# Performance work log

Measured on AMD Instinct MI355X. Metric: run time of the kernel, lower is better.

The kernel has to match this reference:

```python
import jax, jax.numpy as jnp
import numpy as np

C = 1024
H = 16
D = C // H

def setup_inputs() -> dict:
    key = jax.random.key(0)
    ks = jax.random.split(key, 12)
    s = 1.0 / np.sqrt(C)
    inp = {
        "Q": jax.random.normal(ks[0], (2, 1024, C), jnp.float32),
        "K_in": jax.random.normal(ks[1], (2, 4096, C), jnp.float32),
        "V_in": jax.random.normal(ks[2], (2, 4096, C), jnp.float32),
        "V_bias": jax.random.normal(ks[3], (2, 4096), jnp.float32),
        "Wq_w": jax.random.uniform(ks[4], (C, C), jnp.float32, -s, s),
        "Wq_b": jax.random.uniform(ks[5], (C,), jnp.float32, -s, s),
        "Wk_w": jax.random.uniform(ks[6], (C, C), jnp.float32, -s, s),
        "Wk_b": jax.random.uniform(ks[7], (C,), jnp.float32, -s, s),
        "Wv_w": jax.random.uniform(ks[8], (C, C), jnp.float32, -s, s),
        "Wv_b": jax.random.uniform(ks[9], (C,), jnp.float32, -s, s),
        "Wo_w": jax.random.uniform(ks[10], (C, C), jnp.float32, -s, s),
        "Wo_b": jax.random.uniform(ks[11], (C,), jnp.float32, -s, s),
    }
    return inp

def reference(Q, K_in, V_in, V_bias, Wq_w, Wq_b, Wk_w, Wk_b, Wv_w, Wv_b, Wo_w, Wo_b):
    B, Lq, _ = Q.shape
    Lk = K_in.shape[1]
    # linear projections (torch Linear: x @ W.T + b), split heads -> [B,H,L,D]
    q = (Q @ Wq_w.T + Wq_b).reshape(B, Lq, H, D).transpose(0, 2, 1, 3)
    k = (K_in @ Wk_w.T + Wk_b).reshape(B, Lk, H, D).transpose(0, 2, 1, 3)
    v = (V_in @ Wv_w.T + Wv_b).reshape(B, Lk, H, D).transpose(0, 2, 1, 3)
    scale = 1.0 / np.sqrt(D).astype(np.float32)
    logits = jnp.einsum("bhqd,bhkd->bhqk", q, k) * scale
    logits = logits + V_bias[:, None, None, :]  # per-key additive bias
    attn = jax.nn.softmax(logits, axis=-1)      # dropout p=0.0 (eval)
    out = jnp.einsum("bhqk,bhkd->bhqd", attn, v)
    out = out.transpose(0, 2, 1, 3).reshape(B, Lq, C)
    return out @ Wo_w.T + Wo_b
```

## Files before the change

kernel.cpp:

```cpp
#include <hip/hip_runtime.h>


typedef __attribute__((ext_vector_type(8))) __bf16 bf16x8;
typedef __attribute__((ext_vector_type(4))) float f32x4;
typedef __attribute__((ext_vector_type(16))) float f32x16;

#define LOG2E 1.44269504f

__device__ __forceinline__ unsigned short f2bf(float f) {
  union { float f; unsigned u; } v; v.f = f;
  unsigned r = v.u + 0x7fffu + ((v.u >> 16) & 1u);
  return (unsigned short)(r >> 16);
}

__device__ __forceinline__ f32x4 mfma16(bf16x8 a, bf16x8 b, f32x4 c) {
  return __builtin_amdgcn_mfma_f32_16x16x32_bf16(a, b, c, 0, 0, 0);
}
__device__ __forceinline__ f32x16 mfma32(bf16x8 a, bf16x8 b, f32x16 c) {
  return __builtin_amdgcn_mfma_f32_32x32x16_bf16(a, b, c, 0, 0, 0);
}

__device__ __forceinline__ unsigned pk2(float lo, float hi) {
  unsigned short a = __builtin_bit_cast(unsigned short, (__bf16)lo);
  unsigned short b = __builtin_bit_cast(unsigned short, (__bf16)hi);
  return (unsigned)a | ((unsigned)b << 16);
}

struct Cvt4 {
  const float* src[4];
  unsigned short* dst[4];
};

__global__ __launch_bounds__(256) void cvt4_kernel(Cvt4 a, int n4) {
  const float4* s = (const float4*)a.src[blockIdx.y];
  unsigned short* d = a.dst[blockIdx.y];
  int stride = gridDim.x * blockDim.x;
  for (int i = blockIdx.x * blockDim.x + threadIdx.x; i < n4; i += stride) {
    float4 f = s[i];
    ushort4 u;
    u.x = f2bf(f.x); u.y = f2bf(f.y); u.z = f2bf(f.z); u.w = f2bf(f.w);
    ((ushort4*)d)[i] = u;
  }
}

template <int MODE, bool AF32>
__global__ __launch_bounds__(256) void gemm_bf16(
    const void* __restrict__ Ap, const unsigned short* __restrict__ W,
    const float* __restrict__ bias, void* __restrict__ outp,
    int M, int Llog2, float oscale) {
  constexpr int K = 1024, N = 1024;
  __shared__ unsigned short Alds[128][40];
  __shared__ unsigned short Blds[128][40];

  const int tid = threadIdx.x;
  const int wid = tid >> 6, l = tid & 63;
  const int wr = wid >> 1, wc = wid & 1;
  const int m0 = blockIdx.x * 128, n0 = blockIdx.y * 128;
  const int lg = l >> 4, lm = l & 15;

  const int crow = tid >> 2;
  const int ck8 = (tid & 3) * 8;

  const float* Af = (const float*)Ap;
  const unsigned short* Ab = (const unsigned short*)Ap;

  f32x4 acc[4][4] = {};
  uint4 ra[2], rb[2];

  auto loadA = [&](int kt, int half) -> uint4 {
    const int row = crow + half * 64;
    const long off = (long)(m0 + row) * K + kt * 32 + ck8;
    if constexpr (AF32) {
      float4 f0 = *(const float4*)(Af + off);
      float4 f1 = *(const float4*)(Af + off + 4);
      bf16x8 v;
      v[0] = (__bf16)f0.x; v[1] = (__bf16)f0.y;
      v[2] = (__bf16)f0.z; v[3] = (__bf16)f0.w;
      v[4] = (__bf16)f1.x; v[5] = (__bf16)f1.y;
      v[6] = (__bf16)f1.z; v[7] = (__bf16)f1.w;
      uint4 u;
      __builtin_memcpy(&u, &v, 16);
      return u;
    } else {
      return *(const uint4*)(Ab + off);
    }
  };
  auto loadB = [&](int kt, int half) -> uint4 {
    const int row = crow + half * 64;
    return *(const uint4*)(W + (long)(n0 + row) * K + kt * 32 + ck8);
  };

  ra[0] = loadA(0, 0); ra[1] = loadA(0, 1);
  rb[0] = loadB(0, 0); rb[1] = loadB(0, 1);

  for (int kt = 0; kt < K / 32; ++kt) {
    __syncthreads();
    *(uint4*)&Alds[crow][ck8] = ra[0];
    *(uint4*)&Alds[crow + 64][ck8] = ra[1];
    *(uint4*)&Blds[crow][ck8] = rb[0];
    *(uint4*)&Blds[crow + 64][ck8] = rb[1];
    __syncthreads();
    if (kt + 1 < K / 32) {
      ra[0] = loadA(kt + 1, 0); ra[1] = loadA(kt + 1, 1);
      rb[0] = loadB(kt + 1, 0); rb[1] = loadB(kt + 1, 1);
    }
    bf16x8 af[4], bfr[4];
#pragma unroll
    for (int i = 0; i < 4; ++i)
      af[i] = *(const bf16x8*)&Alds[wr * 64 + i * 16 + lm][lg * 8];
#pragma unroll
    for (int j = 0; j < 4; ++j)
      bfr[j] = *(const bf16x8*)&Blds[wc * 64 + j * 16 + lm][lg * 8];
#pragma unroll
    for (int i = 0; i < 4; ++i)
#pragma unroll
      for (int j = 0; j < 4; ++j) {
        if constexpr (MODE == 1)
          acc[i][j] = mfma16(bfr[i], af[j], acc[i][j]);
        else
          acc[i][j] = mfma16(af[i], bfr[j], acc[i][j]);
      }
  }

  const int rr = lg * 4;
  if constexpr (MODE == 0) {
    const int Lmask = (1 << Llog2) - 1;
    unsigned short* out = (unsigned short*)outp;
#pragma unroll
    for (int j = 0; j < 4; ++j) {
      const int n = n0 + wc * 64 + j * 16 + lm;
      const float bv = bias[n];
      const int h = n >> 6, d = n & 63;
#pragma unroll
      for (int i = 0; i < 4; ++i)
#pragma unroll
        for (int r = 0; r < 4; ++r) {
          const int m = m0 + wr * 64 + i * 16 + rr + r;
          const int b = m >> Llog2, li = m & Lmask;
          const long o = (((long)(b * 16 + h) << Llog2) + li) * 64 + d;
          out[o] = f2bf((acc[i][j][r] + bv) * oscale);
        }
    }
  } else if constexpr (MODE == 1) {
    unsigned short* out = (unsigned short*)outp;
#pragma unroll
    for (int i = 0; i < 4; ++i)
#pragma unroll
      for (int r = 0; r < 4; ++r) {
        const int n = n0 + wc * 64 + i * 16 + rr + r;
        const float bv = bias[n];
        const int h = n >> 6, d = n & 63;
#pragma unroll
        for (int j = 0; j < 4; ++j) {
          const int m = m0 + wr * 64 + j * 16 + lm;
          const int b = m >> 12, lk = m & 4095;
          const long o = ((long)((b * 16 + h) * 64 + d)) * 4096 + lk;
          out[o] = f2bf(acc[i][j][r] + bv);
        }
      }
  } else {
    float* out = (float*)outp;
#pragma unroll
    for (int j = 0; j < 4; ++j) {
      const int n = n0 + wc * 64 + j * 16 + lm;
      const float bv = bias[n];
#pragma unroll
      for (int i = 0; i < 4; ++i)
#pragma unroll
        for (int r = 0; r < 4; ++r) {
          const int m = m0 + wr * 64 + i * 16 + rr + r;
          out[(long)m * N + n] = acc[i][j][r] + bv;
        }
    }
  }
}

__global__ __launch_bounds__(256, 2) void attn32(
    const unsigned short* __restrict__ qh, const unsigned short* __restrict__ kh,
    const unsigned short* __restrict__ vT, const float* __restrict__ Vb,
    float* __restrict__ Opart, float* __restrict__ ml) {
  __shared__ unsigned short Klds[2][64][64];
  __shared__ unsigned short Vlds[2][64][64];

  const int tid = threadIdx.x;
  const int wid = tid >> 6, lane = tid & 63;
  const int lq = lane & 31;
  const int hi = lane >> 5;
  const int bh = blockIdx.x;
  const int qb = blockIdx.y;
  const int sp = blockIdx.z;
  const int b = bh >> 4;
  const int q = qb * 128 + wid * 32 + lq;
  const int kt0 = sp * 32;

  bf16x8 qr[4];
  {
    const unsigned short* qp = qh + ((long)bh * 1024 + q) * 64 + hi * 8;
#pragma unroll
    for (int dc = 0; dc < 4; ++dc) qr[dc] = *(const bf16x8*)(qp + dc * 16);
  }

  const int srow = tid >> 2;
  const int ss0 = (tid & 3) * 2, ss1 = ss0 + 1;
  const int sswz = srow & 7;
  const int kgrow = (srow & 0x33) | ((srow & 4) << 1) | ((srow & 8) >> 1);
  const unsigned short* kgp =
      kh + ((long)bh * 4096 + kt0 * 64 + kgrow) * 64;
  const unsigned short* vgp =
      vT + ((long)bh * 64 + srow) * 4096 + kt0 * 64;
  const int ko0 = (ss0 ^ sswz) * 8, ko1 = (ss1 ^ sswz) * 8;
  const float* bp = Vb + b * 4096 + kt0 * 64 + hi * 8;

  uint4 kr0, kr1, vr0, vr1;
  auto loadKV = [&](int t) {
    kr0 = *(const uint4*)(kgp + (long)t * 4096 + ko0);
    kr1 = *(const uint4*)(kgp + (long)t * 4096 + ko1);
    vr0 = *(const uint4*)(vgp + t * 64 + ko0);
    vr1 = *(const uint4*)(vgp + t * 64 + ko1);
  };
  loadKV(0);

  const int rsw = lq & 7;
  float mreg = -1e30f, lreg = 0.f;
  f32x16 oa0 = {}, oa1 = {};

  for (int t = 0; t < 32; ++t) {
    const int buf = t & 1;
    *(uint4*)&Klds[buf][srow][ss0 * 8] = kr0;
    *(uint4*)&Klds[buf][srow][ss1 * 8] = kr1;
    *(uint4*)&Vlds[buf][srow][ss0 * 8] = vr0;
    *(uint4*)&Vlds[buf][srow][ss1 * 8] = vr1;
    if (t + 1 < 32) loadKV(t + 1);

    float bvv[32];
#pragma unroll
    for (int kb = 0; kb < 2; ++kb)
#pragma unroll
      for (int g = 0; g < 4; ++g) {
        float4 t4 = *(const float4*)(bp + t * 64 + kb * 32 + (g & 1) * 4 +
                                     (g >> 1) * 16);
        const int o = kb * 16 + g * 4;
        bvv[o] = t4.x; bvv[o + 1] = t4.y; bvv[o + 2] = t4.z; bvv[o + 3] = t4.w;
      }

    __syncthreads();

    f32x16 sa0 = {}, sa1 = {};
#pragma unroll
    for (int dc = 0; dc < 4; ++dc) {
      const int w16 = dc * 2 + hi;
      bf16x8 kf0 = *(const bf16x8*)&Klds[buf][lq][(w16 ^ rsw) * 8];
      bf16x8 kf1 = *(const bf16x8*)&Klds[buf][32 + lq][(w16 ^ rsw) * 8];
      sa0 = mfma32(kf0, qr[dc], sa0);
      sa1 = mfma32(kf1, qr[dc], sa1);
    }

    float p[32];
#pragma unroll
    for (int r = 0; r < 16; ++r) p[r] = fmaf(bvv[r], LOG2E, sa0[r]);
#pragma unroll
    for (int r = 0; r < 16; ++r) p[16 + r] = fmaf(bvv[16 + r], LOG2E, sa1[r]);

    float t16[16];
#pragma unroll
    for (int i = 0; i < 16; ++i) t16[i] = fmaxf(p[i], p[i + 16]);
#pragma unroll
    for (int s = 8; s > 0; s >>= 1)
#pragma unroll
      for (int i = 0; i < 8; ++i)
        if (i < s) t16[i] = fmaxf(t16[i], t16[i + s]);
    float mx = fmaxf(t16[0], __shfl_xor(t16[0], 32));
    const float mnew = fmaxf(mreg, mx);
    const float al = __builtin_amdgcn_exp2f(mreg - mnew);
    mreg = mnew;
#pragma unroll
    for (int i = 0; i < 32; ++i) p[i] = __builtin_amdgcn_exp2f(p[i] - mreg);
    float s16[16];
#pragma unroll
    for (int i = 0; i < 16; ++i) s16[i] = p[i] + p[i + 16];
#pragma unroll
    for (int s = 8; s > 0; s >>= 1)
#pragma unroll
      for (int i = 0; i < 8; ++i)
        if (i < s) s16[i] += s16[i + s];
    float sm = s16[0] + __shfl_xor(s16[0], 32);
    lreg = lreg * al + sm;
#pragma unroll
    for (int r = 0; r < 16; ++r) { oa0[r] *= al; oa1[r] *= al; }

#pragma unroll
    for (int kc = 0; kc < 4; ++kc) {
      union { uint4 u; bf16x8 v; } pu;
      pu.u = make_uint4(pk2(p[kc * 8 + 0], p[kc * 8 + 1]),
                        pk2(p[kc * 8 + 2], p[kc * 8 + 3]),
                        pk2(p[kc * 8 + 4], p[kc * 8 + 5]),
                        pk2(p[kc * 8 + 6], p[kc * 8 + 7]));
      const int w16 = kc * 2 + hi;
      bf16x8 vf0 = *(const bf16x8*)&Vlds[buf][lq][(w16 ^ rsw) * 8];
      bf16x8 vf1 = *(const bf16x8*)&Vlds[buf][32 + lq][(w16 ^ rsw) * 8];
      oa0 = mfma32(vf0, pu.v, oa0);
      oa1 = mfma32(vf1, pu.v, oa1);
    }
    __syncthreads();
  }

  float* ob = Opart + (((long)sp * 32 + bh) * 1024 + q) * 64;
#pragma unroll
  for (int g = 0; g < 4; ++g) {
    *(float4*)(ob + g * 8 + hi * 4) =
        make_float4(oa0[g * 4], oa0[g * 4 + 1], oa0[g * 4 + 2], oa0[g * 4 + 3]);
    *(float4*)(ob + 32 + g * 8 + hi * 4) =
        make_float4(oa1[g * 4], oa1[g * 4 + 1], oa1[g * 4 + 2], oa1[g * 4 + 3]);
  }
  if (hi == 0)
    *(float2*)(ml + ((long)sp * 32 + bh) * 2048 + q * 2) =
        make_float2(mreg, lreg);
}

__global__ __launch_bounds__(256) void combine_kernel(
    const float* __restrict__ Opart, const float* __restrict__ ml,
    unsigned short* __restrict__ ao) {
  const int idx = blockIdx.x * 256 + threadIdx.x;
  const int bh = idx >> 10, q = idx & 1023;
  const int b = bh >> 4, h = bh & 15;
  const float2 a0 = *(const float2*)(ml + (long)idx * 2);
  const float2 a1 = *(const float2*)(ml + ((long)32768 + idx) * 2);
  const float mm = fmaxf(a0.x, a1.x);
  const float e0 = __builtin_amdgcn_exp2f(a0.x - mm);
  const float e1 = __builtin_amdgcn_exp2f(a1.x - mm);
  const float inv = 1.0f / (a0.y * e0 + a1.y * e1);
  const float s0 = e0 * inv, s1 = e1 * inv;
  const float* O0 = Opart + (long)idx * 64;
  const float* O1 = Opart + ((long)32768 + idx) * 64;
  unsigned short* op = ao + ((long)b * 1024 + q) * 1024 + h * 64;
#pragma unroll
  for (int d = 0; d < 64; d += 4) {
    float4 x = *(const float4*)(O0 + d);
    float4 y = *(const float4*)(O1 + d);
    ushort4 u;
    u.x = f2bf(x.x * s0 + y.x * s1);
    u.y = f2bf(x.y * s0 + y.y * s1);
    u.z = f2bf(x.z * s0 + y.z * s1);
    u.w = f2bf(x.w * s0 + y.w * s1);
    *(ushort4*)(op + d) = u;
  }
}

extern "C" void kernel_launch(void* const* d_in, const int* in_sizes, int n_in,
                              void* d_out, int out_size, void* d_ws,
                              size_t ws_size, hipStream_t stream) {
  const float* Q = (const float*)d_in[0];
  const float* K_in = (const float*)d_in[1];
  const float* V_in = (const float*)d_in[2];
  const float* V_bias = (const float*)d_in[3];
  const float* Wq_w = (const float*)d_in[4];
  const float* Wq_b = (const float*)d_in[5];
  const float* Wk_w = (const float*)d_in[6];
  const float* Wk_b = (const float*)d_in[7];
  const float* Wv_w = (const float*)d_in[8];
  const float* Wv_b = (const float*)d_in[9];
  const float* Wo_w = (const float*)d_in[10];
  const float* Wo_b = (const float*)d_in[11];

  char* ws = (char*)d_ws;
  unsigned short* Wqb = (unsigned short*)(ws + (0l << 20));
  unsigned short* Wkb = (unsigned short*)(ws + (2l << 20));
  unsigned short* Wvb = (unsigned short*)(ws + (4l << 20));
  unsigned short* Wob = (unsigned short*)(ws + (6l << 20));
  unsigned short* qhp = (unsigned short*)(ws + (8l << 20));
  unsigned short* khp = (unsigned short*)(ws + (12l << 20));
  unsigned short* vTp = (unsigned short*)(ws + (28l << 20));
  float* Opart = (float*)(ws + (44l << 20));
  unsigned short* aop = (unsigned short*)(ws + (60l << 20));
  float* mlp = (float*)(ws + (64l << 20));

  Cvt4 c4;
  c4.src[0] = Wq_w; c4.src[1] = Wk_w; c4.src[2] = Wv_w; c4.src[3] = Wo_w;
  c4.dst[0] = Wqb;  c4.dst[1] = Wkb;  c4.dst[2] = Wvb;  c4.dst[3] = Wob;
  cvt4_kernel<<<dim3(256, 4), 256, 0, stream>>>(c4, (1024 * 1024) / 4);

  gemm_bf16<0, true><<<dim3(16, 8), 256, 0, stream>>>(
      Q, Wqb, Wq_b, qhp, 2048, 10, 0.125f * LOG2E);
  gemm_bf16<0, true><<<dim3(64, 8), 256, 0, stream>>>(
      K_in, Wkb, Wk_b, khp, 8192, 12, 1.0f);
  gemm_bf16<1, true><<<dim3(64, 8), 256, 0, stream>>>(
      V_in, Wvb, Wv_b, vTp, 8192, 12, 1.0f);

  attn32<<<dim3(32, 8, 2), 256, 0, stream>>>(qhp, khp, vTp, V_bias, Opart, mlp);
  combine_kernel<<<128, 256, 0, stream>>>(Opart, mlp, aop);

  gemm_bf16<2, false><<<dim3(16, 8), 256, 0, stream>>>(
      aop, Wob, Wo_b, d_out, 2048, 0, 1.0f);
}
```

Baseline: 187.8 us.

## Rework attention: async LDS loads, MFMA bias and rowsum, lazy rescale, 4-way split

The attention kernel now loads K/V tiles straight into LDS with global_load_lds instead of staging them through registers. The per-key bias is pre-scaled and split into hi/lo bf16 pairs, then added through an extra MFMA. The softmax row sum is also computed with an MFMA against ones, and rescaling is skipped unless the running max grows by more than 8. The key range is split four ways instead of two, occupancy is raised to 3 blocks per CU, and partial outputs are normalised and stored as fp16 so the combine kernel reads less data. The risks are a small precision loss from fp16 partials and the bf16 bias split, and extra small kernels and MFMAs per tile.

Result: no change. 188.7 us (+0.5%).

```diff
diff --git a/kernel.cpp b/kernel.cpp
--- a/kernel.cpp
+++ b/kernel.cpp
@@ -12,6 +12,13 @@
   unsigned r = v.u + 0x7fffu + ((v.u >> 16) & 1u);
   return (unsigned short)(r >> 16);
 }
+__device__ __forceinline__ unsigned short f2h(float x) {
+  _Float16 h = (_Float16)x;
+  return __builtin_bit_cast(unsigned short, h);
+}
+__device__ __forceinline__ float h2f(unsigned short u) {
+  return (float)__builtin_bit_cast(_Float16, u);
+}
 
 __device__ __forceinline__ f32x4 mfma16(bf16x8 a, bf16x8 b, f32x4 c) {
   return __builtin_amdgcn_mfma_f32_16x16x32_bf16(a, b, c, 0, 0, 0);
@@ -24,6 +31,13 @@
   unsigned short a = __builtin_bit_cast(unsigned short, (__bf16)lo);
   unsigned short b = __builtin_bit_cast(unsigned short, (__bf16)hi);
   return (unsigned)a | ((unsigned)b << 16);
+}
+
+template <typename T>
+__device__ __forceinline__ void gload16(const T* g, T* l) {
+  __builtin_amdgcn_global_load_lds(
+      (const __attribute__((address_space(1))) void*)g,
+      (__attribute__((address_space(3))) void*)l, 16, 0, 0);
 }
 
 struct Cvt4 {
@@ -41,6 +55,16 @@
     u.x = f2bf(f.x); u.y = f2bf(f.y); u.z = f2bf(f.z); u.w = f2bf(f.w);
     ((ushort4*)d)[i] = u;
   }
+}
+
+__global__ __launch_bounds__(256) void prep_kb(const float* __restrict__ Vb,
+                                               unsigned* __restrict__ kb) {
+  const int i = blockIdx.x * 256 + threadIdx.x;
+  const float x = Vb[i] * LOG2E;
+  const unsigned short h = f2bf(x);
+  union { unsigned u; float f; } hf; hf.u = (unsigned)h << 16;
+  const unsigned short lo = f2bf(x - hf.f);
+  kb[i] = (unsigned)h | ((unsigned)lo << 16);
 }
 
 template <int MODE, bool AF32>
@@ -175,23 +199,20 @@
   }
 }
 
-__global__ __launch_bounds__(256, 2) void attn32(
+__global__ __launch_bounds__(256, 3) void attn32(
     const unsigned short* __restrict__ qh, const unsigned short* __restrict__ kh,
-    const unsigned short* __restrict__ vT, const float* __restrict__ Vb,
-    float* __restrict__ Opart, float* __restrict__ ml) {
+    const unsigned short* __restrict__ vT, const unsigned* __restrict__ kb,
+    unsigned short* __restrict__ Oh, float* __restrict__ ml) {
   __shared__ unsigned short Klds[2][64][64];
   __shared__ unsigned short Vlds[2][64][64];
 
   const int tid = threadIdx.x;
   const int wid = tid >> 6, lane = tid & 63;
-  const int lq = lane & 31;
-  const int hi = lane >> 5;
-  const int bh = blockIdx.x;
-  const int qb = blockIdx.y;
-  const int sp = blockIdx.z;
+  const int lq = lane & 31, hi = lane >> 5;
+  const int bh = blockIdx.x, qb = blockIdx.y, sp = blockIdx.z;
   const int b = bh >> 4;
   const int q = qb * 128 + wid * 32 + lq;
-  const int kt0 = sp * 32;
+  const int kt0 = sp * 16;
 
   bf16x8 qr[4];
   {
@@ -200,149 +221,162 @@
     for (int dc = 0; dc < 4; ++dc) qr[dc] = *(const bf16x8*)(qp + dc * 16);
   }
 
-  const int srow = tid >> 2;
-  const int ss0 = (tid & 3) * 2, ss1 = ss0 + 1;
-  const int sswz = srow & 7;
-  const int kgrow = (srow & 0x33) | ((srow & 4) << 1) | ((srow & 8) >> 1);
-  const unsigned short* kgp =
-      kh + ((long)bh * 4096 + kt0 * 64 + kgrow) * 64;
-  const unsigned short* vgp =
-      vT + ((long)bh * 64 + srow) * 4096 + kt0 * 64;
-  const int ko0 = (ss0 ^ sswz) * 8, ko1 = (ss1 ^ sswz) * 8;
-  const float* bp = Vb + b * 4096 + kt0 * 64 + hi * 8;
-
-  uint4 kr0, kr1, vr0, vr1;
-  auto loadKV = [&](int t) {
-    kr0 = *(const uint4*)(kgp + (long)t * 4096 + ko0);
-    kr1 = *(const uint4*)(kgp + (long)t * 4096 + ko1);
-    vr0 = *(const uint4*)(vgp + t * 64 + ko0);
-    vr1 = *(const uint4*)(vgp + t * 64 + ko1);
+  union uv { uint4 u; bf16x8 v; };
+  uv ones; ones.u = make_uint4(0x3F803F80u, 0x3F803F80u, 0x3F803F80u, 0x3F803F80u);
+  uv bq;   bq.u = make_uint4(hi ? 0u : 0x3F803F80u, 0u, 0u, 0u);
+
+  auto swap23 = [](int r) { return (r & 0x33) | ((r & 4) << 1) | ((r & 8) >> 1); };
+  const int r0 = wid * 16 + (lane >> 3), r1 = r0 + 8;
+  const int s0 = ((lane & 7) ^ (r0 & 7)) * 8;
+  const int s1 = ((lane & 7) ^ (r1 & 7)) * 8;
+  const unsigned short* kg0 =
+      kh + ((long)bh * 4096 + kt0 * 64 + swap23(r0)) * 64 + s0;
+  const unsigned short* kg1 =
+      kh + ((long)bh * 4096 + kt0 * 64 + swap23(r1)) * 64 + s1;
+  const unsigned short* vg0 = vT + ((long)bh * 64 + r0) * 4096 + kt0 * 64 + s0;
+  const unsigned short* vg1 = vT + ((long)bh * 64 + r1) * 4096 + kt0 * 64 + s1;
+  const unsigned* kbp = kb + b * 4096 + kt0 * 64;
+  const int kbkey = swap23(lq);
+
+  auto issue = [&](int t, int buf) {
+    gload16(kg0 + (long)t * 4096, &Klds[buf][wid * 16][0]);
+    gload16(kg1 + (long)t * 4096, &Klds[buf][wid * 16 + 8][0]);
+    gload16(vg0 + t * 64, &Vlds[buf][wid * 16][0]);
+    gload16(vg1 + t * 64, &Vlds[buf][wid * 16 + 8][0]);
   };
-  loadKV(0);
+  issue(0, 0);
 
   const int rsw = lq & 7;
-  float mreg = -1e30f, lreg = 0.f;
-  f32x16 oa0 = {}, oa1 = {};
-
-  for (int t = 0; t < 32; ++t) {
+  float mreg = -1e30f;
+  f32x16 oa0 = {}, oa1 = {}, lacc = {};
+
+  for (int t = 0; t < 16; ++t) {
     const int buf = t & 1;
-    *(uint4*)&Klds[buf][srow][ss0 * 8] = kr0;
-    *(uint4*)&Klds[buf][srow][ss1 * 8] = kr1;
-    *(uint4*)&Vlds[buf][srow][ss0 * 8] = vr0;
-    *(uint4*)&Vlds[buf][srow][ss1 * 8] = vr1;
-    if (t + 1 < 32) loadKV(t + 1);
-
-    float bvv[32];
-#pragma unroll
-    for (int kb = 0; kb < 2; ++kb)
-#pragma unroll
-      for (int g = 0; g < 4; ++g) {
-        float4 t4 = *(const float4*)(bp + t * 64 + kb * 32 + (g & 1) * 4 +
-                                     (g >> 1) * 16);
-        const int o = kb * 16 + g * 4;
-        bvv[o] = t4.x; bvv[o + 1] = t4.y; bvv[o + 2] = t4.z; bvv[o + 3] = t4.w;
-      }
-
     __syncthreads();
+    if (t + 1 < 16) issue(t + 1, buf ^ 1);
+
+    const unsigned kbw0 = kbp[t * 64 + kbkey];
+    const unsigned kbw1 = kbp[t * 64 + 32 + kbkey];
 
     f32x16 sa0 = {}, sa1 = {};
+    __builtin_amdgcn_s_setprio(1);
 #pragma unroll
     for (int dc = 0; dc < 4; ++dc) {
-      const int w16 = dc * 2 + hi;
-      bf16x8 kf0 = *(const bf16x8*)&Klds[buf][lq][(w16 ^ rsw) * 8];
-      bf16x8 kf1 = *(const bf16x8*)&Klds[buf][32 + lq][(w16 ^ rsw) * 8];
+      const int so = ((dc * 2 + hi) ^ rsw) * 8;
+      bf16x8 kf0 = *(const bf16x8*)&Klds[buf][lq][so];
+      bf16x8 kf1 = *(const bf16x8*)&Klds[buf][32 + lq][so];
       sa0 = mfma32(kf0, qr[dc], sa0);
       sa1 = mfma32(kf1, qr[dc], sa1);
     }
+    {
+      uv ka0, ka1;
+      ka0.u = make_uint4(hi ? 0u : kbw0, 0u, 0u, 0u);
+      ka1.u = make_uint4(hi ? 0u : kbw1, 0u, 0u, 0u);
+      sa0 = mfma32(ka0.v, bq.v, sa0);
+      sa1 = mfma32(ka1.v, bq.v, sa1);
+    }
+    __builtin_amdgcn_s_setprio(0);
 
     float p[32];
 #pragma unroll
-    for (int r = 0; r < 16; ++r) p[r] = fmaf(bvv[r], LOG2E, sa0[r]);
-#pragma unroll
-    for (int r = 0; r < 16; ++r) p[16 + r] = fmaf(bvv[16 + r], LOG2E, sa1[r]);
-
-    float t16[16];
-#pragma unroll
-    for (int i = 0; i < 16; ++i) t16[i] = fmaxf(p[i], p[i + 16]);
-#pragma unroll
-    for (int s = 8; s > 0; s >>= 1)
-#pragma unroll
-      for (int i = 0; i < 8; ++i)
-        if (i < s) t16[i] = fmaxf(t16[i], t16[i + s]);
-    float mx = fmaxf(t16[0], __shfl_xor(t16[0], 32));
-    const float mnew = fmaxf(mreg, mx);
-    const float al = __builtin_amdgcn_exp2f(mreg - mnew);
-    mreg = mnew;
+    for (int r = 0; r < 16; ++r) { p[r] = sa0[r]; p[16 + r] = sa1[r]; }
+
+    float t8[8];
+#pragma unroll
+    for (int i = 0; i < 8; ++i)
+      t8[i] = fmaxf(fmaxf(p[i], p[i + 8]), fmaxf(p[i + 16], p[i + 24]));
+    float mx = fmaxf(fmaxf(fmaxf(t8[0], t8[1]), fmaxf(t8[2], t8[3])),
+                     fmaxf(fmaxf(t8[4], t8[5]), fmaxf(t8[6], t8[7])));
+    mx = fmaxf(mx, __shfl_xor(mx, 32));
+
+    if (!__all(mx - mreg <= 8.0f)) {
+      const float mnew = fmaxf(mreg, mx);
+      const float al = __builtin_amdgcn_exp2f(mreg - mnew);
+      mreg = mnew;
+#pragma unroll
+      for (int r = 0; r < 16; ++r) { oa0[r] *= al; oa1[r] *= al; }
+      lacc[0] *= al;
+    }
 #pragma unroll
     for (int i = 0; i < 32; ++i) p[i] = __builtin_amdgcn_exp2f(p[i] - mreg);
-    float s16[16];
-#pragma unroll
-    for (int i = 0; i < 16; ++i) s16[i] = p[i] + p[i + 16];
-#pragma unroll
-    for (int s = 8; s > 0; s >>= 1)
-#pragma unroll
-      for (int i = 0; i < 8; ++i)
-        if (i < s) s16[i] += s16[i + s];
-    float sm = s16[0] + __shfl_xor(s16[0], 32);
-    lreg = lreg * al + sm;
-#pragma unroll
-    for (int r = 0; r < 16; ++r) { oa0[r] *= al; oa1[r] *= al; }
-
+
+    __builtin_amdgcn_s_setprio(1);
 #pragma unroll
     for (int kc = 0; kc < 4; ++kc) {
-      union { uint4 u; bf16x8 v; } pu;
+      uv pu;
       pu.u = make_uint4(pk2(p[kc * 8 + 0], p[kc * 8 + 1]),
                         pk2(p[kc * 8 + 2], p[kc * 8 + 3]),
                         pk2(p[kc * 8 + 4], p[kc * 8 + 5]),
                         pk2(p[kc * 8 + 6], p[kc * 8 + 7]));
-      const int w16 = kc * 2 + hi;
-      bf16x8 vf0 = *(const bf16x8*)&Vlds[buf][lq][(w16 ^ rsw) * 8];
-      bf16x8 vf1 = *(const bf16x8*)&Vlds[buf][32 + lq][(w16 ^ rsw) * 8];
+      const int so = ((kc * 2 + hi) ^ rsw) * 8;
+      bf16x8 vf0 = *(const bf16x8*)&Vlds[buf][lq][so];
+      bf16x8 vf1 = *(const bf16x8*)&Vlds[buf][32 + lq][so];
       oa0 = mfma32(vf0, pu.v, oa0);
       oa1 = mfma32(vf1, pu.v, oa1);
-    }
-    __syncthreads();
-  }
-
-  float* ob = Opart + (((long)sp * 32 + bh) * 1024 + q) * 64;
+      lacc = mfma32(ones.v, pu.v, lacc);
+    }
+    __builtin_amdgcn_s_setprio(0);
+  }
+
+  const float lsum = lacc[0];
+  const float inv = 1.0f / lsum;
+  unsigned short* ob = Oh + (((long)sp * 32 + bh) * 1024 + q) * 64 + hi * 4;
 #pragma unroll
   for (int g = 0; g < 4; ++g) {
-    *(float4*)(ob + g * 8 + hi * 4) =
-        make_float4(oa0[g * 4], oa0[g * 4 + 1], oa0[g * 4 + 2], oa0[g * 4 + 3]);
-    *(float4*)(ob + 32 + g * 8 + hi * 4) =
-        make_float4(oa1[g * 4], oa1[g * 4 + 1], oa1[g * 4 + 2], oa1[g * 4 + 3]);
+    ushort4 u0, u1;
+    u0.x = f2h(oa0[g * 4 + 0] * inv); u0.y = f2h(oa0[g * 4 + 1] * inv);
+    u0.z = f2h(oa0[g * 4 + 2] * inv); u0.w = f2h(oa0[g * 4 + 3] * inv);
+    u1.x = f2h(oa1[g * 4 + 0] * inv); u1.y = f2h(oa1[g * 4 + 1] * inv);
+    u1.z = f2h(oa1[g * 4 + 2] * inv); u1.w = f2h(oa1[g * 4 + 3] * inv);
+    *(ushort4*)(ob + g * 8) = u0;
+    *(ushort4*)(ob + 32 + g * 8) = u1;
   }
   if (hi == 0)
-    *(float2*)(ml + ((long)sp * 32 + bh) * 2048 + q * 2) =
-        make_float2(mreg, lreg);
-}
-
-__global__ __launch_bounds__(256) void combine_kernel(
-    const float* __restrict__ Opart, const float* __restrict__ ml,
+    *(float2*)(ml + (((long)sp * 32 + bh) * 1024 + q) * 2) =
+        make_float2(mreg, lsum);
+}
+
+__global__ __launch_bounds__(256) void combine4(
+    const unsigned short* __restrict__ Oh, const float* __restrict__ ml,
     unsigned short* __restrict__ ao) {
   const int idx = blockIdx.x * 256 + threadIdx.x;
   const int bh = idx >> 10, q = idx & 1023;
   const int b = bh >> 4, h = bh & 15;
-  const float2 a0 = *(const float2*)(ml + (long)idx * 2);
-  const float2 a1 = *(const float2*)(ml + ((long)32768 + idx) * 2);
-  const float mm = fmaxf(a0.x, a1.x);
-  const float e0 = __builtin_amdgcn_exp2f(a0.x - mm);
-  const float e1 = __builtin_amdgcn_exp2f(a1.x - mm);
-  const float inv = 1.0f / (a0.y * e0 + a1.y * e1);
-  const float s0 = e0 * inv, s1 = e1 * inv;
-  const float* O0 = Opart + (long)idx * 64;
-  const float* O1 = Opart + ((long)32768 + idx) * 64;
+  float m[4], l[4];
+#pragma unroll
+  for (int i = 0; i < 4; ++i) {
+    float2 t = *(const float2*)(ml + ((long)i * 32768 + idx) * 2);
+    m[i] = t.x; l[i] = t.y;
+  }
+  const float mm = fmaxf(fmaxf(m[0], m[1]), fmaxf(m[2], m[3]));
+  float w[4], wsum = 0.f;
+#pragma unroll
+  for (int i = 0; i < 4; ++i) {
+    w[i] = l[i] * __builtin_amdgcn_exp2f(m[i] - mm);
+    wsum += w[i];
+  }
+  const float inv = 1.0f / wsum;
+#pragma unroll
+  for (int i = 0; i < 4; ++i) w[i] *= inv;
+
   unsigned short* op = ao + ((long)b * 1024 + q) * 1024 + h * 64;
 #pragma unroll
-  for (int d = 0; d < 64; d += 4) {
-    float4 x = *(const float4*)(O0 + d);
-    float4 y = *(const float4*)(O1 + d);
-    ushort4 u;
-    u.x = f2bf(x.x * s0 + y.x * s1);
-    u.y = f2bf(x.y * s0 + y.y * s1);
-    u.z = f2bf(x.z * s0 + y.z * s1);
-    u.w = f2bf(x.w * s0 + y.w * s1);
-    *(ushort4*)(op + d) = u;
+  for (int blk = 0; blk < 8; ++blk) {
+    float acc[8] = {};
+#pragma unroll
+    for (int i = 0; i < 4; ++i) {
+      uint4 u = *(const uint4*)(Oh + ((long)i * 32768 + idx) * 64 + blk * 8);
+      const unsigned short* hs = (const unsigned short*)&u;
+#pragma unroll
+      for (int j = 0; j < 8; ++j) acc[j] += w[i] * h2f(hs[j]);
+    }
+    ushort4 o0, o1;
+    o0.x = f2bf(acc[0]); o0.y = f2bf(acc[1]);
+    o0.z = f2bf(acc[2]); o0.w = f2bf(acc[3]);
+    o1.x = f2bf(acc[4]); o1.y = f2bf(acc[5]);
+    o1.z = f2bf(acc[6]); o1.w = f2bf(acc[7]);
+    *(ushort4*)(op + blk * 8) = o0;
+    *(ushort4*)(op + blk * 8 + 4) = o1;
   }
 }
 
@@ -364,20 +398,22 @@
 
   char* ws = (char*)d_ws;
   unsigned short* Wqb = (unsigned short*)(ws + (0l << 20));
+  float* mlp = (float*)(ws + (0l << 20));
   unsigned short* Wkb = (unsigned short*)(ws + (2l << 20));
   unsigned short* Wvb = (unsigned short*)(ws + (4l << 20));
   unsigned short* Wob = (unsigned short*)(ws + (6l << 20));
   unsigned short* qhp = (unsigned short*)(ws + (8l << 20));
   unsigned short* khp = (unsigned short*)(ws + (12l << 20));
   unsigned short* vTp = (unsigned short*)(ws + (28l << 20));
-  float* Opart = (float*)(ws + (44l << 20));
+  unsigned short* Ohp = (unsigned short*)(ws + (44l << 20));
   unsigned short* aop = (unsigned short*)(ws + (60l << 20));
-  float* mlp = (float*)(ws + (64l << 20));
+  unsigned* kbp = (unsigned*)(ws + (64l << 20));
 
   Cvt4 c4;
   c4.src[0] = Wq_w; c4.src[1] = Wk_w; c4.src[2] = Wv_w; c4.src[3] = Wo_w;
   c4.dst[0] = Wqb;  c4.dst[1] = Wkb;  c4.dst[2] = Wvb;  c4.dst[3] = Wob;
   cvt4_kernel<<<dim3(256, 4), 256, 0, stream>>>(c4, (1024 * 1024) / 4);
+  prep_kb<<<32, 256, 0, stream>>>(V_bias, kbp);
 
   gemm_bf16<0, true><<<dim3(16, 8), 256, 0, stream>>>(
       Q, Wqb, Wq_b, qhp, 2048, 10, 0.125f * LOG2E);
@@ -386,8 +422,8 @@
   gemm_bf16<1, true><<<dim3(64, 8), 256, 0, stream>>>(
       V_in, Wvb, Wv_b, vTp, 8192, 12, 1.0f);
 
-  attn32<<<dim3(32, 8, 2), 256, 0, stream>>>(qhp, khp, vTp, V_bias, Opart, mlp);
-  combine_kernel<<<128, 256, 0, stream>>>(Opart, mlp, aop);
+  attn32<<<dim3(32, 8, 4), 256, 0, stream>>>(qhp, khp, vTp, kbp, Ohp, mlp);
+  combine4<<<128, 256, 0, stream>>>(Ohp, mlp, aop);
 
   gemm_bf16<2, false><<<dim3(16, 8), 256, 0, stream>>>(
       aop, Wob, Wo_b, d_out, 2048, 0, 1.0f);
```
